# Kernel tuning notes

Measured on AMD Instinct MI355X. Metric: run time of the kernel, lower is better.

The kernel has to match this reference:

```python
import jax, jax.numpy as jnp
import numpy as np

G, S, M = 131072, 16, 8  # num_groups, state_dim, measure_dim


def setup_inputs() -> dict:
    key = jax.random.key(0)
    ks = jax.random.split(key, 7)
    inp = jax.random.normal(ks[0], (G, M), jnp.float32)
    mean = jax.random.normal(ks[1], (G, S), jnp.float32)
    a = jax.random.normal(ks[2], (G, S, S), jnp.float32)
    cov = a @ jnp.swapaxes(a, -1, -2) / S + jnp.eye(S, dtype=jnp.float32)  # SPD state cov
    H = jax.random.normal(ks[3], (G, M, S), jnp.float32) * 0.5
    b = jax.random.normal(ks[4], (G, M, M), jnp.float32)
    R = b @ jnp.swapaxes(b, -1, -2) / M + jnp.eye(M, dtype=jnp.float32)  # SPD measure noise
    F = jax.random.normal(ks[5], (G, S, S), jnp.float32) * (0.5 / np.sqrt(S))  # quasi-stable transition
    c = jax.random.normal(ks[6], (G, S, S), jnp.float32)
    Q = c @ jnp.swapaxes(c, -1, -2) / S + 0.1 * jnp.eye(S, dtype=jnp.float32)  # SPD process noise
    return {"input": inp, "mean": mean, "cov": cov, "H": H, "R": R, "F": F, "Q": Q}


def reference(input, mean, cov, H, R, F, Q):
    # --- update (no-NaN path of GaussianStep.update -> _update) ---
    Ht = jnp.swapaxes(H, -1, -2)                     # [G,S,M]
    covHt = cov @ Ht                                 # [G,S,M]
    Ssys = H @ covHt + R                             # innovation covariance [G,M,M]
    # torch: solve(B=covHt^T, A=Ssys^T) then transpose -> K = covHt @ inv(Ssys)
    Kt = jnp.linalg.solve(jnp.swapaxes(Ssys, -1, -2), jnp.swapaxes(covHt, -1, -2))  # [G,M,S]
    K = jnp.swapaxes(Kt, -1, -2)                     # [G,S,M]
    resid = input - jnp.einsum('gms,gs->gm', H, mean)
    new_mean = mean + jnp.einsum('gsm,gm->gs', K, resid)
    I = jnp.eye(S, dtype=cov.dtype)
    ikh = I - K @ H                                  # [G,S,S]
    # stable (Joseph form) covariance update
    new_cov = ikh @ cov @ jnp.swapaxes(ikh, -1, -2) + K @ R @ jnp.swapaxes(K, -1, -2)
    # --- predict ---
    pred_mean = jnp.einsum('gij,gj->gi', F, new_mean)
    pred_cov = F @ new_cov @ jnp.swapaxes(F, -1, -2) + Q
    return pred_mean, pred_cov
```

## Files before the change

### kernel.cpp

```cpp
#include <hip/hip_runtime.h>


typedef float v2f __attribute__((ext_vector_type(2)));
typedef _Float16 h2 __attribute__((ext_vector_type(2)));

__device__ __forceinline__ float bq(float x, int t) {
    switch (t & 3) {
    case 0:  return __int_as_float(__builtin_amdgcn_mov_dpp(__float_as_int(x), 0x00, 0xF, 0xF, true));
    case 1:  return __int_as_float(__builtin_amdgcn_mov_dpp(__float_as_int(x), 0x55, 0xF, 0xF, true));
    case 2:  return __int_as_float(__builtin_amdgcn_mov_dpp(__float_as_int(x), 0xAA, 0xF, 0xF, true));
    default: return __int_as_float(__builtin_amdgcn_mov_dpp(__float_as_int(x), 0xFF, 0xF, 0xF, true));
    }
}
__device__ __forceinline__ v2f splat(float c) { v2f r; r.x = c; r.y = c; return r; }
__device__ __forceinline__ v2f up2(h2 h) { v2f r; r.x = (float)h.x; r.y = (float)h.y; return r; }

__global__ __launch_bounds__(64) void kalman_kernel(
    const float* __restrict__ g_in,
    const float* __restrict__ g_mean,
    const float* __restrict__ g_cov,
    const float* __restrict__ g_H,
    const float* __restrict__ g_R,
    const float* __restrict__ g_F,
    const float* __restrict__ g_Q,
    float* __restrict__ g_out,
    int G)
{
    const int l = threadIdx.x & 3;
    const int g = (blockIdx.x << 4) | (threadIdx.x >> 2);

    const float* const Pp = g_cov + (size_t)g * 256;
    const float* const Hp = g_H   + (size_t)g * 128;
    const float* const Rp = g_R   + (size_t)g * 64;
    const float* const Fp = g_F   + (size_t)g * 256;
    const float* const Qp = g_Q   + (size_t)g * 256;

    v2f Plo[16], Phi[16];
    #pragma unroll
    for (int k = 0; k < 16; ++k) {
        const float4 t = *reinterpret_cast<const float4*>(Pp + k*16 + 4*l);
        Plo[k].x=t.x; Plo[k].y=t.y; Phi[k].x=t.z; Phi[k].y=t.w;
    }
    h2 HT16[16];
    {
        float4 ra[4], rb[4];
        #pragma unroll
        for (int p = 0; p < 4; ++p) {
            ra[p] = *reinterpret_cast<const float4*>(Hp + (2*l  )*16 + 4*p);
            rb[p] = *reinterpret_cast<const float4*>(Hp + (2*l+1)*16 + 4*p);
        }
        #pragma unroll
        for (int p = 0; p < 4; ++p) {
            HT16[4*p+0].x=(_Float16)ra[p].x; HT16[4*p+0].y=(_Float16)rb[p].x;
            HT16[4*p+1].x=(_Float16)ra[p].y; HT16[4*p+1].y=(_Float16)rb[p].y;
            HT16[4*p+2].x=(_Float16)ra[p].z; HT16[4*p+2].y=(_Float16)rb[p].z;
            HT16[4*p+3].x=(_Float16)ra[p].w; HT16[4*p+3].y=(_Float16)rb[p].w;
        }
    }
    v2f S[8];
    #pragma unroll
    for (int i = 0; i < 8; ++i) {
        const float2 t = *reinterpret_cast<const float2*>(Rp + i*8 + 2*l);
        S[i].x=t.x; S[i].y=t.y;
    }
    v2f mnlo, mnhi;
    { const float4 t = *reinterpret_cast<const float4*>(g_mean + (size_t)g*16 + 4*l);
      mnlo.x=t.x; mnlo.y=t.y; mnhi.x=t.z; mnhi.y=t.w; }
    v2f ipv;
    { const float2 t = *reinterpret_cast<const float2*>(g_in + (size_t)g*8 + 2*l);
      ipv.x=t.x; ipv.y=t.y; }

    v2f CTlo[8], CThi[8];
    #pragma unroll
    for (int i = 0; i < 8; ++i) {
        v2f alo = {0.f, 0.f}, ahi = {0.f, 0.f};
        #pragma unroll
        for (int k = 0; k < 16; ++k) {
            const float h = bq((float)((i&1) ? HT16[k].y : HT16[k].x), i>>1);
            alo += splat(h) * Plo[k];
            ahi += splat(h) * Phi[k];
        }
        CTlo[i]=alo; CThi[i]=ahi;
    }

    #pragma unroll
    for (int i = 0; i < 8; ++i) {
        v2f acc = S[i];
        #pragma unroll
        for (int k = 0; k < 16; ++k) {
            const float c = bq((k&2) ? ((k&1)?CThi[i].y:CThi[i].x)
                                     : ((k&1)?CTlo[i].y:CTlo[i].x), k>>2);
            acc += splat(c) * up2(HT16[k]);
        }
        S[i] = acc;
    }

    v2f resd = ipv;
    #pragma unroll
    for (int k = 0; k < 16; ++k) {
        const float m = bq((k&2) ? ((k&1)?mnhi.y:mnhi.x)
                                 : ((k&1)?mnlo.y:mnlo.x), k>>2);
        resd -= splat(m) * up2(HT16[k]);
    }

    v2f Ii[8];
    #pragma unroll
    for (int i = 0; i < 8; ++i) {
        Ii[i].x = (2*l   == i) ? 1.f : 0.f;
        Ii[i].y = (2*l+1 == i) ? 1.f : 0.f;
    }
    #pragma unroll
    for (int k = 0; k < 8; ++k) {
        const float pv   = bq((k&1) ? S[k].y : S[k].x, k>>1);
        const float pinv = __builtin_amdgcn_rcpf(pv);
        S[k]  *= splat(pinv);
        Ii[k] *= splat(pinv);
        #pragma unroll
        for (int i = 0; i < 8; ++i) {
            if (i == k) continue;
            const float fi = bq((k&1) ? S[i].y : S[i].x, k>>1);
            S[i]  -= splat(fi) * S[k];
            Ii[i] -= splat(fi) * Ii[k];
        }
    }

    h2 FT16a[16], FT16b[16];
    {
        #pragma unroll
        for (int p = 0; p < 4; ++p) {
            const float4 r0 = *reinterpret_cast<const float4*>(Fp + (4*l+0)*16 + 4*p);
            const float4 r1 = *reinterpret_cast<const float4*>(Fp + (4*l+1)*16 + 4*p);
            const float4 r2 = *reinterpret_cast<const float4*>(Fp + (4*l+2)*16 + 4*p);
            const float4 r3 = *reinterpret_cast<const float4*>(Fp + (4*l+3)*16 + 4*p);
            FT16a[4*p+0].x=(_Float16)r0.x; FT16a[4*p+0].y=(_Float16)r1.x;
            FT16b[4*p+0].x=(_Float16)r2.x; FT16b[4*p+0].y=(_Float16)r3.x;
            FT16a[4*p+1].x=(_Float16)r0.y; FT16a[4*p+1].y=(_Float16)r1.y;
            FT16b[4*p+1].x=(_Float16)r2.y; FT16b[4*p+1].y=(_Float16)r3.y;
            FT16a[4*p+2].x=(_Float16)r0.z; FT16a[4*p+2].y=(_Float16)r1.z;
            FT16b[4*p+2].x=(_Float16)r2.z; FT16b[4*p+2].y=(_Float16)r3.z;
            FT16a[4*p+3].x=(_Float16)r0.w; FT16a[4*p+3].y=(_Float16)r1.w;
            FT16b[4*p+3].x=(_Float16)r2.w; FT16b[4*p+3].y=(_Float16)r3.w;
        }
    }

    v2f nmL = mnlo, nmH = mnhi;
    #pragma unroll
    for (int m = 0; m < 8; ++m) {
        v2f xlo = {0.f,0.f}, xhi = {0.f,0.f};
        #pragma unroll
        for (int j = 0; j < 8; ++j) {
            const float s = bq((j&1) ? Ii[m].y : Ii[m].x, j>>1);
            xlo += splat(s) * CTlo[j];
            xhi += splat(s) * CThi[j];
        }
        const float r = bq((m&1) ? resd.y : resd.x, m>>1);
        nmL += splat(r) * xlo;
        nmH += splat(r) * xhi;
        #pragma unroll
        for (int s2 = 0; s2 < 16; ++s2) {
            const float c = bq((s2&2) ? ((s2&1)?CThi[m].y:CThi[m].x)
                                      : ((s2&1)?CTlo[m].y:CTlo[m].x), s2>>2);
            Plo[s2] -= splat(c) * xlo;
            Phi[s2] -= splat(c) * xhi;
        }
    }

    {
        v2f plo = {0.f,0.f}, phi = {0.f,0.f};
        #pragma unroll
        for (int k = 0; k < 16; ++k) {
            const float m = bq((k&2) ? ((k&1)?nmH.y:nmH.x)
                                     : ((k&1)?nmL.y:nmL.x), k>>2);
            plo += splat(m) * up2(FT16a[k]);
            phi += splat(m) * up2(FT16b[k]);
        }
        *reinterpret_cast<float4*>(g_out + (size_t)g*16 + 4*l) =
            make_float4(plo.x, plo.y, phi.x, phi.y);
    }

    float* const out_pc = g_out + (size_t)G*16 + (size_t)g*256;
    #pragma unroll
    for (int i = 0; i < 16; ++i) {
        const float4 qv = *reinterpret_cast<const float4*>(Qp + i*16 + 4*l);
        v2f wlo = {0.f,0.f}, whi = {0.f,0.f};
        #pragma unroll
        for (int k = 0; k < 16; ++k) {
            const float f = bq((float)((i&2) ? ((i&1)?FT16b[k].y:FT16b[k].x)
                                             : ((i&1)?FT16a[k].y:FT16a[k].x)), i>>2);
            wlo += splat(f) * Plo[k];
            whi += splat(f) * Phi[k];
        }
        v2f olo; olo.x=qv.x; olo.y=qv.y;
        v2f ohi; ohi.x=qv.z; ohi.y=qv.w;
        #pragma unroll
        for (int t = 0; t < 16; ++t) {
            const float wb = bq((t&2) ? ((t&1)?whi.y:whi.x)
                                      : ((t&1)?wlo.y:wlo.x), t>>2);
            olo += splat(wb) * up2(FT16a[t]);
            ohi += splat(wb) * up2(FT16b[t]);
        }
        *reinterpret_cast<float4*>(out_pc + i*16 + 4*l) =
            make_float4(olo.x, olo.y, ohi.x, ohi.y);
    }
}

extern "C" void kernel_launch(void* const* d_in, const int* in_sizes, int n_in,
                              void* d_out, int out_size, void* d_ws, size_t ws_size,
                              hipStream_t stream) {
    const float* g_in   = (const float*)d_in[0];
    const float* g_mean = (const float*)d_in[1];
    const float* g_cov  = (const float*)d_in[2];
    const float* g_H    = (const float*)d_in[3];
    const float* g_R    = (const float*)d_in[4];
    const float* g_F    = (const float*)d_in[5];
    const float* g_Q    = (const float*)d_in[6];
    float* out = (float*)d_out;
    const int G = in_sizes[2] / 256;
    kalman_kernel<<<G/16, 64, 0, stream>>>(g_in, g_mean, g_cov, g_H, g_R, g_F, g_Q, out, G);
}
```

Baseline: 158.3 us.

## Process two groups per thread quad with software-prefetched loads for second group

Each block now handles 32 groups: every thread quad processes group A, then group B, and during group A's output loop it prefetches group B's cov, H, R, mean and input into registers, with sched barriers placing the loads. Q is also loaded through a 5-deep rotating register buffer, and H is kept in fp32 instead of being converted to fp16. The aim is to hide global-load latency behind compute and cut launch overhead. The cost is much higher register pressure, which may lower occupancy or cause spills, and half as many blocks.

```diff
diff --git a/kernel.cpp b/kernel.cpp
--- a/kernel.cpp
+++ b/kernel.cpp
@@ -26,181 +26,375 @@
     float* __restrict__ g_out,
     int G)
 {
-    const int l = threadIdx.x & 3;
-    const int g = (blockIdx.x << 4) | (threadIdx.x >> 2);
-
-    const float* const Pp = g_cov + (size_t)g * 256;
-    const float* const Hp = g_H   + (size_t)g * 128;
-    const float* const Rp = g_R   + (size_t)g * 64;
-    const float* const Fp = g_F   + (size_t)g * 256;
-    const float* const Qp = g_Q   + (size_t)g * 256;
-
-    v2f Plo[16], Phi[16];
-    #pragma unroll
-    for (int k = 0; k < 16; ++k) {
-        const float4 t = *reinterpret_cast<const float4*>(Pp + k*16 + 4*l);
-        Plo[k].x=t.x; Plo[k].y=t.y; Phi[k].x=t.z; Phi[k].y=t.w;
+    const int l  = threadIdx.x & 3;
+    const int gA = (blockIdx.x << 5) | (threadIdx.x >> 2);
+    const int gB = gA + 16;
+
+    float4 tPB[16];
+    float4 tHaB[4], tHbB[4];
+    float2 tSB[8];
+    float4 tmnB;
+    float2 tipB;
+
+    float* const out_pc_base = g_out + (size_t)G * 16;
+
+    {
+        const float* const Pp = g_cov + (size_t)gA * 256;
+        const float* const Hp = g_H   + (size_t)gA * 128;
+        const float* const Rp = g_R   + (size_t)gA * 64;
+        const float* const Fp = g_F   + (size_t)gA * 256;
+        const float* const Qp = g_Q   + (size_t)gA * 256;
+
+        v2f Plo[16], Phi[16];
+        #pragma unroll
+        for (int k = 0; k < 16; ++k) {
+            const float4 t = *reinterpret_cast<const float4*>(Pp + k*16 + 4*l);
+            Plo[k].x=t.x; Plo[k].y=t.y; Phi[k].x=t.z; Phi[k].y=t.w;
+        }
+        v2f HT[16];
+        {
+            float4 ra[4], rb[4];
+            #pragma unroll
+            for (int p = 0; p < 4; ++p) {
+                ra[p] = *reinterpret_cast<const float4*>(Hp + (2*l  )*16 + 4*p);
+                rb[p] = *reinterpret_cast<const float4*>(Hp + (2*l+1)*16 + 4*p);
+            }
+            #pragma unroll
+            for (int p = 0; p < 4; ++p) {
+                HT[4*p+0].x=ra[p].x; HT[4*p+0].y=rb[p].x;
+                HT[4*p+1].x=ra[p].y; HT[4*p+1].y=rb[p].y;
+                HT[4*p+2].x=ra[p].z; HT[4*p+2].y=rb[p].z;
+                HT[4*p+3].x=ra[p].w; HT[4*p+3].y=rb[p].w;
+            }
+        }
+        v2f S[8];
+        #pragma unroll
+        for (int i = 0; i < 8; ++i) {
+            const float2 t = *reinterpret_cast<const float2*>(Rp + i*8 + 2*l);
+            S[i].x=t.x; S[i].y=t.y;
+        }
+        v2f mnlo, mnhi;
+        { const float4 t = *reinterpret_cast<const float4*>(g_mean + (size_t)gA*16 + 4*l);
+          mnlo.x=t.x; mnlo.y=t.y; mnhi.x=t.z; mnhi.y=t.w; }
+        v2f ipv;
+        { const float2 t = *reinterpret_cast<const float2*>(g_in + (size_t)gA*8 + 2*l);
+          ipv.x=t.x; ipv.y=t.y; }
+
+        v2f CTlo[8], CThi[8];
+        #pragma unroll
+        for (int i = 0; i < 8; ++i) {
+            v2f alo = {0.f,0.f}, ahi = {0.f,0.f};
+            #pragma unroll
+            for (int k = 0; k < 16; ++k) {
+                const float h = bq((i&1) ? HT[k].y : HT[k].x, i>>1);
+                alo += splat(h) * Plo[k];
+                ahi += splat(h) * Phi[k];
+            }
+            CTlo[i]=alo; CThi[i]=ahi;
+        }
+        #pragma unroll
+        for (int i = 0; i < 8; ++i) {
+            v2f acc = S[i];
+            #pragma unroll
+            for (int k = 0; k < 16; ++k) {
+                const float c = bq((k&2) ? ((k&1)?CThi[i].y:CThi[i].x)
+                                         : ((k&1)?CTlo[i].y:CTlo[i].x), k>>2);
+                acc += splat(c) * HT[k];
+            }
+            S[i] = acc;
+        }
+        v2f resd = ipv;
+        #pragma unroll
+        for (int k = 0; k < 16; ++k) {
+            const float m = bq((k&2) ? ((k&1)?mnhi.y:mnhi.x)
+                                     : ((k&1)?mnlo.y:mnlo.x), k>>2);
+            resd -= splat(m) * HT[k];
+        }
+        v2f Ii[8];
+        #pragma unroll
+        for (int i = 0; i < 8; ++i) {
+            Ii[i].x = (2*l   == i) ? 1.f : 0.f;
+            Ii[i].y = (2*l+1 == i) ? 1.f : 0.f;
+        }
+        #pragma unroll
+        for (int k = 0; k < 8; ++k) {
+            const float pv   = bq((k&1) ? S[k].y : S[k].x, k>>1);
+            const float pinv = __builtin_amdgcn_rcpf(pv);
+            S[k]  *= splat(pinv);
+            Ii[k] *= splat(pinv);
+            #pragma unroll
+            for (int i = 0; i < 8; ++i) {
+                if (i == k) continue;
+                const float fi = bq((k&1) ? S[i].y : S[i].x, k>>1);
+                S[i]  -= splat(fi) * S[k];
+                Ii[i] -= splat(fi) * Ii[k];
+            }
+        }
+        h2 FT16a[16], FT16b[16];
+        {
+            #pragma unroll
+            for (int p = 0; p < 4; ++p) {
+                const float4 r0 = *reinterpret_cast<const float4*>(Fp + (4*l+0)*16 + 4*p);
+                const float4 r1 = *reinterpret_cast<const float4*>(Fp + (4*l+1)*16 + 4*p);
+                const float4 r2 = *reinterpret_cast<const float4*>(Fp + (4*l+2)*16 + 4*p);
+                const float4 r3 = *reinterpret_cast<const float4*>(Fp + (4*l+3)*16 + 4*p);
+                FT16a[4*p+0].x=(_Float16)r0.x; FT16a[4*p+0].y=(_Float16)r1.x;
+                FT16b[4*p+0].x=(_Float16)r2.x; FT16b[4*p+0].y=(_Float16)r3.x;
+                FT16a[4*p+1].x=(_Float16)r0.y; FT16a[4*p+1].y=(_Float16)r1.y;
+                FT16b[4*p+1].x=(_Float16)r2.y; FT16b[4*p+1].y=(_Float16)r3.y;
+                FT16a[4*p+2].x=(_Float16)r0.z; FT16a[4*p+2].y=(_Float16)r1.z;
+                FT16b[4*p+2].x=(_Float16)r2.z; FT16b[4*p+2].y=(_Float16)r3.z;
+                FT16a[4*p+3].x=(_Float16)r0.w; FT16a[4*p+3].y=(_Float16)r1.w;
+                FT16b[4*p+3].x=(_Float16)r2.w; FT16b[4*p+3].y=(_Float16)r3.w;
+            }
+        }
+        float4 qbuf[5];
+        #pragma unroll
+        for (int i = 0; i < 5; ++i)
+            qbuf[i] = *reinterpret_cast<const float4*>(Qp + i*16 + 4*l);
+
+        v2f nmL = mnlo, nmH = mnhi;
+        #pragma unroll
+        for (int m = 0; m < 8; ++m) {
+            v2f xlo = {0.f,0.f}, xhi = {0.f,0.f};
+            #pragma unroll
+            for (int j = 0; j < 8; ++j) {
+                const float s = bq((j&1) ? Ii[m].y : Ii[m].x, j>>1);
+                xlo += splat(s) * CTlo[j];
+                xhi += splat(s) * CThi[j];
+            }
+            const float r = bq((m&1) ? resd.y : resd.x, m>>1);
+            nmL += splat(r) * xlo;
+            nmH += splat(r) * xhi;
+            #pragma unroll
+            for (int s2 = 0; s2 < 16; ++s2) {
+                const float c = bq((s2&2) ? ((s2&1)?CThi[m].y:CThi[m].x)
+                                          : ((s2&1)?CTlo[m].y:CTlo[m].x), s2>>2);
+                Plo[s2] -= splat(c) * xlo;
+                Phi[s2] -= splat(c) * xhi;
+            }
+        }
+        {
+            v2f plo = {0.f,0.f}, phi = {0.f,0.f};
+            #pragma unroll
+            for (int k = 0; k < 16; ++k) {
+                const float m = bq((k&2) ? ((k&1)?nmH.y:nmH.x)
+                                         : ((k&1)?nmL.y:nmL.x), k>>2);
+                plo += splat(m) * up2(FT16a[k]);
+                phi += splat(m) * up2(FT16b[k]);
+            }
+            *reinterpret_cast<float4*>(g_out + (size_t)gA*16 + 4*l) =
+                make_float4(plo.x, plo.y, phi.x, phi.y);
+        }
+        const float* const PpB = g_cov + (size_t)gB * 256;
+        const float* const HpB = g_H   + (size_t)gB * 128;
+        const float* const RpB = g_R   + (size_t)gB * 64;
+        float* const out_pc = out_pc_base + (size_t)gA*256;
+        #pragma unroll
+        for (int i = 0; i < 16; ++i) {
+            v2f wlo = {0.f,0.f}, whi = {0.f,0.f};
+            #pragma unroll
+            for (int k = 0; k < 16; ++k) {
+                const float f = bq((float)((i&2) ? ((i&1)?FT16b[k].y:FT16b[k].x)
+                                                 : ((i&1)?FT16a[k].y:FT16a[k].x)), i>>2);
+                wlo += splat(f) * Plo[k];
+                whi += splat(f) * Phi[k];
+            }
+            const float4 qv = qbuf[i % 5];
+            if (i + 5 < 16)
+                qbuf[i % 5] = *reinterpret_cast<const float4*>(Qp + (i+5)*16 + 4*l);
+            v2f olo; olo.x=qv.x; olo.y=qv.y;
+            v2f ohi; ohi.x=qv.z; ohi.y=qv.w;
+            #pragma unroll
+            for (int t = 0; t < 16; ++t) {
+                const float wb = bq((t&2) ? ((t&1)?whi.y:whi.x)
+                                          : ((t&1)?wlo.y:wlo.x), t>>2);
+                olo += splat(wb) * up2(FT16a[t]);
+                ohi += splat(wb) * up2(FT16b[t]);
+            }
+            *reinterpret_cast<float4*>(out_pc + i*16 + 4*l) =
+                make_float4(olo.x, olo.y, ohi.x, ohi.y);
+            if (i == 2) {
+                #pragma unroll
+                for (int k = 0; k < 16; ++k)
+                    tPB[k] = *reinterpret_cast<const float4*>(PpB + k*16 + 4*l);
+                __builtin_amdgcn_sched_barrier(0);
+            }
+            if (i == 6) {
+                #pragma unroll
+                for (int p = 0; p < 4; ++p) {
+                    tHaB[p] = *reinterpret_cast<const float4*>(HpB + (2*l  )*16 + 4*p);
+                    tHbB[p] = *reinterpret_cast<const float4*>(HpB + (2*l+1)*16 + 4*p);
+                }
+                __builtin_amdgcn_sched_barrier(0);
+            }
+            if (i == 10) {
+                #pragma unroll
+                for (int r = 0; r < 8; ++r)
+                    tSB[r] = *reinterpret_cast<const float2*>(RpB + r*8 + 2*l);
+                tmnB = *reinterpret_cast<const float4*>(g_mean + (size_t)gB*16 + 4*l);
+                tipB = *reinterpret_cast<const float2*>(g_in + (size_t)gB*8 + 2*l);
+                __builtin_amdgcn_sched_barrier(0);
+            }
+        }
     }
-    h2 HT16[16];
+
     {
-        float4 ra[4], rb[4];
+        const float* const Fp = g_F + (size_t)gB * 256;
+        const float* const Qp = g_Q + (size_t)gB * 256;
+
+        v2f Plo[16], Phi[16];
+        #pragma unroll
+        for (int k = 0; k < 16; ++k) {
+            Plo[k].x=tPB[k].x; Plo[k].y=tPB[k].y; Phi[k].x=tPB[k].z; Phi[k].y=tPB[k].w;
+        }
+        v2f HT[16];
         #pragma unroll
         for (int p = 0; p < 4; ++p) {
-            ra[p] = *reinterpret_cast<const float4*>(Hp + (2*l  )*16 + 4*p);
-            rb[p] = *reinterpret_cast<const float4*>(Hp + (2*l+1)*16 + 4*p);
-        }
-        #pragma unroll
-        for (int p = 0; p < 4; ++p) {
-            HT16[4*p+0].x=(_Float16)ra[p].x; HT16[4*p+0].y=(_Float16)rb[p].x;
-            HT16[4*p+1].x=(_Float16)ra[p].y; HT16[4*p+1].y=(_Float16)rb[p].y;
-            HT16[4*p+2].x=(_Float16)ra[p].z; HT16[4*p+2].y=(_Float16)rb[p].z;
-            HT16[4*p+3].x=(_Float16)ra[p].w; HT16[4*p+3].y=(_Float16)rb[p].w;
-        }
-    }
-    v2f S[8];
-    #pragma unroll
-    for (int i = 0; i < 8; ++i) {
-        const float2 t = *reinterpret_cast<const float2*>(Rp + i*8 + 2*l);
-        S[i].x=t.x; S[i].y=t.y;
-    }
-    v2f mnlo, mnhi;
-    { const float4 t = *reinterpret_cast<const float4*>(g_mean + (size_t)g*16 + 4*l);
-      mnlo.x=t.x; mnlo.y=t.y; mnhi.x=t.z; mnhi.y=t.w; }
-    v2f ipv;
-    { const float2 t = *reinterpret_cast<const float2*>(g_in + (size_t)g*8 + 2*l);
-      ipv.x=t.x; ipv.y=t.y; }
-
-    v2f CTlo[8], CThi[8];
-    #pragma unroll
-    for (int i = 0; i < 8; ++i) {
-        v2f alo = {0.f, 0.f}, ahi = {0.f, 0.f};
+            HT[4*p+0].x=tHaB[p].x; HT[4*p+0].y=tHbB[p].x;
+            HT[4*p+1].x=tHaB[p].y; HT[4*p+1].y=tHbB[p].y;
+            HT[4*p+2].x=tHaB[p].z; HT[4*p+2].y=tHbB[p].z;
+            HT[4*p+3].x=tHaB[p].w; HT[4*p+3].y=tHbB[p].w;
+        }
+        v2f S[8];
+        #pragma unroll
+        for (int i = 0; i < 8; ++i) { S[i].x=tSB[i].x; S[i].y=tSB[i].y; }
+        v2f mnlo, mnhi;
+        mnlo.x=tmnB.x; mnlo.y=tmnB.y; mnhi.x=tmnB.z; mnhi.y=tmnB.w;
+        v2f ipv; ipv.x=tipB.x; ipv.y=tipB.y;
+
+        v2f CTlo[8], CThi[8];
+        #pragma unroll
+        for (int i = 0; i < 8; ++i) {
+            v2f alo = {0.f,0.f}, ahi = {0.f,0.f};
+            #pragma unroll
+            for (int k = 0; k < 16; ++k) {
+                const float h = bq((i&1) ? HT[k].y : HT[k].x, i>>1);
+                alo += splat(h) * Plo[k];
+                ahi += splat(h) * Phi[k];
+            }
+            CTlo[i]=alo; CThi[i]=ahi;
+        }
+        #pragma unroll
+        for (int i = 0; i < 8; ++i) {
+            v2f acc = S[i];
+            #pragma unroll
+            for (int k = 0; k < 16; ++k) {
+                const float c = bq((k&2) ? ((k&1)?CThi[i].y:CThi[i].x)
+                                         : ((k&1)?CTlo[i].y:CTlo[i].x), k>>2);
+                acc += splat(c) * HT[k];
+            }
+            S[i] = acc;
+        }
+        v2f resd = ipv;
         #pragma unroll
         for (int k = 0; k < 16; ++k) {
-            const float h = bq((float)((i&1) ? HT16[k].y : HT16[k].x), i>>1);
-            alo += splat(h) * Plo[k];
-            ahi += splat(h) * Phi[k];
-        }
-        CTlo[i]=alo; CThi[i]=ahi;
-    }
-
-    #pragma unroll
-    for (int i = 0; i < 8; ++i) {
-        v2f acc = S[i];
-        #pragma unroll
-        for (int k = 0; k < 16; ++k) {
-            const float c = bq((k&2) ? ((k&1)?CThi[i].y:CThi[i].x)
-                                     : ((k&1)?CTlo[i].y:CTlo[i].x), k>>2);
-            acc += splat(c) * up2(HT16[k]);
-        }
-        S[i] = acc;
-    }
-
-    v2f resd = ipv;
-    #pragma unroll
-    for (int k = 0; k < 16; ++k) {
-        const float m = bq((k&2) ? ((k&1)?mnhi.y:mnhi.x)
-                                 : ((k&1)?mnlo.y:mnlo.x), k>>2);
-        resd -= splat(m) * up2(HT16[k]);
-    }
-
-    v2f Ii[8];
-    #pragma unroll
-    for (int i = 0; i < 8; ++i) {
-        Ii[i].x = (2*l   == i) ? 1.f : 0.f;
-        Ii[i].y = (2*l+1 == i) ? 1.f : 0.f;
-    }
-    #pragma unroll
-    for (int k = 0; k < 8; ++k) {
-        const float pv   = bq((k&1) ? S[k].y : S[k].x, k>>1);
-        const float pinv = __builtin_amdgcn_rcpf(pv);
-        S[k]  *= splat(pinv);
-        Ii[k] *= splat(pinv);
-        #pragma unroll
-        for (int i = 0; i < 8; ++i) {
-            if (i == k) continue;
-            const float fi = bq((k&1) ? S[i].y : S[i].x, k>>1);
-            S[i]  -= splat(fi) * S[k];
-            Ii[i] -= splat(fi) * Ii[k];
-        }
-    }
-
-    h2 FT16a[16], FT16b[16];
-    {
-        #pragma unroll
-        for (int p = 0; p < 4; ++p) {
-            const float4 r0 = *reinterpret_cast<const float4*>(Fp + (4*l+0)*16 + 4*p);
-            const float4 r1 = *reinterpret_cast<const float4*>(Fp + (4*l+1)*16 + 4*p);
-            const float4 r2 = *reinterpret_cast<const float4*>(Fp + (4*l+2)*16 + 4*p);
-            const float4 r3 = *reinterpret_cast<const float4*>(Fp + (4*l+3)*16 + 4*p);
-            FT16a[4*p+0].x=(_Float16)r0.x; FT16a[4*p+0].y=(_Float16)r1.x;
-            FT16b[4*p+0].x=(_Float16)r2.x; FT16b[4*p+0].y=(_Float16)r3.x;
-            FT16a[4*p+1].x=(_Float16)r0.y; FT16a[4*p+1].y=(_Float16)r1.y;
-            FT16b[4*p+1].x=(_Float16)r2.y; FT16b[4*p+1].y=(_Float16)r3.y;
-            FT16a[4*p+2].x=(_Float16)r0.z; FT16a[4*p+2].y=(_Float16)r1.z;
-            FT16b[4*p+2].x=(_Float16)r2.z; FT16b[4*p+2].y=(_Float16)r3.z;
-            FT16a[4*p+3].x=(_Float16)r0.w; FT16a[4*p+3].y=(_Float16)r1.w;
-            FT16b[4*p+3].x=(_Float16)r2.w; FT16b[4*p+3].y=(_Float16)r3.w;
-        }
-    }
-
-    v2f nmL = mnlo, nmH = mnhi;
-    #pragma unroll
-    for (int m = 0; m < 8; ++m) {
-        v2f xlo = {0.f,0.f}, xhi = {0.f,0.f};
-        #pragma unroll
-        for (int j = 0; j < 8; ++j) {
-            const float s = bq((j&1) ? Ii[m].y : Ii[m].x, j>>1);
-            xlo += splat(s) * CTlo[j];
-            xhi += splat(s) * CThi[j];
-        }
-        const float r = bq((m&1) ? resd.y : resd.x, m>>1);
-        nmL += splat(r) * xlo;
-        nmH += splat(r) * xhi;
-        #pragma unroll
-        for (int s2 = 0; s2 < 16; ++s2) {
-            const float c = bq((s2&2) ? ((s2&1)?CThi[m].y:CThi[m].x)
-                                      : ((s2&1)?CTlo[m].y:CTlo[m].x), s2>>2);
-            Plo[s2] -= splat(c) * xlo;
-            Phi[s2] -= splat(c) * xhi;
-        }
-    }
-
-    {
-        v2f plo = {0.f,0.f}, phi = {0.f,0.f};
-        #pragma unroll
-        for (int k = 0; k < 16; ++k) {
-            const float m = bq((k&2) ? ((k&1)?nmH.y:nmH.x)
-                                     : ((k&1)?nmL.y:nmL.x), k>>2);
-            plo += splat(m) * up2(FT16a[k]);
-            phi += splat(m) * up2(FT16b[k]);
-        }
-        *reinterpret_cast<float4*>(g_out + (size_t)g*16 + 4*l) =
-            make_float4(plo.x, plo.y, phi.x, phi.y);
-    }
-
-    float* const out_pc = g_out + (size_t)G*16 + (size_t)g*256;
-    #pragma unroll
-    for (int i = 0; i < 16; ++i) {
-        const float4 qv = *reinterpret_cast<const float4*>(Qp + i*16 + 4*l);
-        v2f wlo = {0.f,0.f}, whi = {0.f,0.f};
-        #pragma unroll
-        for (int k = 0; k < 16; ++k) {
-            const float f = bq((float)((i&2) ? ((i&1)?FT16b[k].y:FT16b[k].x)
-                                             : ((i&1)?FT16a[k].y:FT16a[k].x)), i>>2);
-            wlo += splat(f) * Plo[k];
-            whi += splat(f) * Phi[k];
-        }
-        v2f olo; olo.x=qv.x; olo.y=qv.y;
-        v2f ohi; ohi.x=qv.z; ohi.y=qv.w;
-        #pragma unroll
-        for (int t = 0; t < 16; ++t) {
-            const float wb = bq((t&2) ? ((t&1)?whi.y:whi.x)
-                                      : ((t&1)?wlo.y:wlo.x), t>>2);
-            olo += splat(wb) * up2(FT16a[t]);
-            ohi += splat(wb) * up2(FT16b[t]);
-        }
-        *reinterpret_cast<float4*>(out_pc + i*16 + 4*l) =
-            make_float4(olo.x, olo.y, ohi.x, ohi.y);
+            const float m = bq((k&2) ? ((k&1)?mnhi.y:mnhi.x)
+                                     : ((k&1)?mnlo.y:mnlo.x), k>>2);
+            resd -= splat(m) * HT[k];
+        }
+        v2f Ii[8];
+        #pragma unroll
+        for (int i = 0; i < 8; ++i) {
+            Ii[i].x = (2*l   == i) ? 1.f : 0.f;
+            Ii[i].y = (2*l+1 == i) ? 1.f : 0.f;
+        }
+        #pragma unroll
+        for (int k = 0; k < 8; ++k) {
+            const float pv   = bq((k&1) ? S[k].y : S[k].x, k>>1);
+            const float pinv = __builtin_amdgcn_rcpf(pv);
+            S[k]  *= splat(pinv);
+            Ii[k] *= splat(pinv);
+            #pragma unroll
+            for (int i = 0; i < 8; ++i) {
+                if (i == k) continue;
+                const float fi = bq((k&1) ? S[i].y : S[i].x, k>>1);
+                S[i]  -= splat(fi) * S[k];
+                Ii[i] -= splat(fi) * Ii[k];
+            }
+        }
+        h2 FT16a[16], FT16b[16];
+        {
+            #pragma unroll
+            for (int p = 0; p < 4; ++p) {
+                const float4 r0 = *reinterpret_cast<const float4*>(Fp + (4*l+0)*16 + 4*p);
+                const float4 r1 = *reinterpret_cast<const float4*>(Fp + (4*l+1)*16 + 4*p);
+                const float4 r2 = *reinterpret_cast<const float4*>(Fp + (4*l+2)*16 + 4*p);
+                const float4 r3 = *reinterpret_cast<const float4*>(Fp + (4*l+3)*16 + 4*p);
+                FT16a[4*p+0].x=(_Float16)r0.x; FT16a[4*p+0].y=(_Float16)r1.x;
+                FT16b[4*p+0].x=(_Float16)r2.x; FT16b[4*p+0].y=(_Float16)r3.x;
+                FT16a[4*p+1].x=(_Float16)r0.y; FT16a[4*p+1].y=(_Float16)r1.y;
+                FT16b[4*p+1].x=(_Float16)r2.y; FT16b[4*p+1].y=(_Float16)r3.y;
+                FT16a[4*p+2].x=(_Float16)r0.z; FT16a[4*p+2].y=(_Float16)r1.z;
+                FT16b[4*p+2].x=(_Float16)r2.z; FT16b[4*p+2].y=(_Float16)r3.z;
+                FT16a[4*p+3].x=(_Float16)r0.w; FT16a[4*p+3].y=(_Float16)r1.w;
+                FT16b[4*p+3].x=(_Float16)r2.w; FT16b[4*p+3].y=(_Float16)r3.w;
+            }
+        }
+        float4 qbuf[5];
+        #pragma unroll
+        for (int i = 0; i < 5; ++i)
+            qbuf[i] = *reinterpret_cast<const float4*>(Qp + i*16 + 4*l);
+
+        v2f nmL = mnlo, nmH = mnhi;
+        #pragma unroll
+        for (int m = 0; m < 8; ++m) {
+            v2f xlo = {0.f,0.f}, xhi = {0.f,0.f};
+            #pragma unroll
+            for (int j = 0; j < 8; ++j) {
+                const float s = bq((j&1) ? Ii[m].y : Ii[m].x, j>>1);
+                xlo += splat(s) * CTlo[j];
+                xhi += splat(s) * CThi[j];
+            }
+            const float r = bq((m&1) ? resd.y : resd.x, m>>1);
+            nmL += splat(r) * xlo;
+            nmH += splat(r) * xhi;
+            #pragma unroll
+            for (int s2 = 0; s2 < 16; ++s2) {
+                const float c = bq((s2&2) ? ((s2&1)?CThi[m].y:CThi[m].x)
+                                          : ((s2&1)?CTlo[m].y:CTlo[m].x), s2>>2);
+                Plo[s2] -= splat(c) * xlo;
+                Phi[s2] -= splat(c) * xhi;
+            }
+        }
+        {
+            v2f plo = {0.f,0.f}, phi = {0.f,0.f};
+            #pragma unroll
+            for (int k = 0; k < 16; ++k) {
+                const float m = bq((k&2) ? ((k&1)?nmH.y:nmH.x)
+                                         : ((k&1)?nmL.y:nmL.x), k>>2);
+                plo += splat(m) * up2(FT16a[k]);
+                phi += splat(m) * up2(FT16b[k]);
+            }
+            *reinterpret_cast<float4*>(g_out + (size_t)gB*16 + 4*l) =
+                make_float4(plo.x, plo.y, phi.x, phi.y);
+        }
+        float* const out_pc = out_pc_base + (size_t)gB*256;
+        #pragma unroll
+        for (int i = 0; i < 16; ++i) {
+            v2f wlo = {0.f,0.f}, whi = {0.f,0.f};
+            #pragma unroll
+            for (int k = 0; k < 16; ++k) {
+                const float f = bq((float)((i&2) ? ((i&1)?FT16b[k].y:FT16b[k].x)
+                                                 : ((i&1)?FT16a[k].y:FT16a[k].x)), i>>2);
+                wlo += splat(f) * Plo[k];
+                whi += splat(f) * Phi[k];
+            }
+            const float4 qv = qbuf[i % 5];
+            if (i + 5 < 16)
+                qbuf[i % 5] = *reinterpret_cast<const float4*>(Qp + (i+5)*16 + 4*l);
+            v2f olo; olo.x=qv.x; olo.y=qv.y;
+            v2f ohi; ohi.x=qv.z; ohi.y=qv.w;
+            #pragma unroll
+            for (int t = 0; t < 16; ++t) {
+                const float wb = bq((t&2) ? ((t&1)?whi.y:whi.x)
+                                          : ((t&1)?wlo.y:wlo.x), t>>2);
+                olo += splat(wb) * up2(FT16a[t]);
+                ohi += splat(wb) * up2(FT16b[t]);
+            }
+            *reinterpret_cast<float4*>(out_pc + i*16 + 4*l) =
+                make_float4(olo.x, olo.y, ohi.x, ohi.y);
+        }
     }
 }
 
@@ -216,5 +410,5 @@
     const float* g_Q    = (const float*)d_in[6];
     float* out = (float*)d_out;
     const int G = in_sizes[2] / 256;
-    kalman_kernel<<<G/16, 64, 0, stream>>>(g_in, g_mean, g_cov, g_H, g_R, g_F, g_Q, out, G);
+    kalman_kernel<<<G/32, 64, 0, stream>>>(g_in, g_mean, g_cov, g_H, g_R, g_F, g_Q, out, G);
 }
```

Result: faster. 140.2 us (-11.4%).

## Invert innovation matrix in place and reorder loads to cut register pressure

Applied to the files above, without the earlier changes.

Replaces the separate Gauss-Jordan identity array with in-place inversion inside S, so the explicit inverse shares storage with the matrix being reduced. The residual is computed early and the mean reloaded later instead of being held live. R is loaded lazily, a sched_barrier keeps the F loads after the update phase, and Q rows are prefetched two ahead. The aim is fewer live VGPRs, which may allow higher occupancy or avoid spills. The cost is some extra select instructions and a repeated mean load.

```diff
diff --git a/kernel.cpp b/kernel.cpp
--- a/kernel.cpp
+++ b/kernel.cpp
@@ -57,23 +57,22 @@
             HT16[4*p+3].x=(_Float16)ra[p].w; HT16[4*p+3].y=(_Float16)rb[p].w;
         }
     }
-    v2f S[8];
+    v2f resd;
+    {
+        const float2 it = *reinterpret_cast<const float2*>(g_in + (size_t)g*8 + 2*l);
+        const float4 mt = *reinterpret_cast<const float4*>(g_mean + (size_t)g*16 + 4*l);
+        resd.x = it.x; resd.y = it.y;
+        #pragma unroll
+        for (int k = 0; k < 16; ++k) {
+            const float m = bq((k&2) ? ((k&1)?mt.w:mt.z) : ((k&1)?mt.y:mt.x), k>>2);
+            resd -= splat(m) * up2(HT16[k]);
+        }
+    }
+
+    v2f CTlo[8], CThi[8];
     #pragma unroll
     for (int i = 0; i < 8; ++i) {
-        const float2 t = *reinterpret_cast<const float2*>(Rp + i*8 + 2*l);
-        S[i].x=t.x; S[i].y=t.y;
-    }
-    v2f mnlo, mnhi;
-    { const float4 t = *reinterpret_cast<const float4*>(g_mean + (size_t)g*16 + 4*l);
-      mnlo.x=t.x; mnlo.y=t.y; mnhi.x=t.z; mnhi.y=t.w; }
-    v2f ipv;
-    { const float2 t = *reinterpret_cast<const float2*>(g_in + (size_t)g*8 + 2*l);
-      ipv.x=t.x; ipv.y=t.y; }
-
-    v2f CTlo[8], CThi[8];
-    #pragma unroll
-    for (int i = 0; i < 8; ++i) {
-        v2f alo = {0.f, 0.f}, ahi = {0.f, 0.f};
+        v2f alo = {0.f,0.f}, ahi = {0.f,0.f};
         #pragma unroll
         for (int k = 0; k < 16; ++k) {
             const float h = bq((float)((i&1) ? HT16[k].y : HT16[k].x), i>>1);
@@ -83,9 +82,11 @@
         CTlo[i]=alo; CThi[i]=ahi;
     }
 
+    v2f S[8];
     #pragma unroll
     for (int i = 0; i < 8; ++i) {
-        v2f acc = S[i];
+        const float2 rt = *reinterpret_cast<const float2*>(Rp + i*8 + 2*l);
+        v2f acc; acc.x = rt.x; acc.y = rt.y;
         #pragma unroll
         for (int k = 0; k < 16; ++k) {
             const float c = bq((k&2) ? ((k&1)?CThi[i].y:CThi[i].x)
@@ -95,34 +96,50 @@
         S[i] = acc;
     }
 
-    v2f resd = ipv;
-    #pragma unroll
-    for (int k = 0; k < 16; ++k) {
-        const float m = bq((k&2) ? ((k&1)?mnhi.y:mnhi.x)
-                                 : ((k&1)?mnlo.y:mnlo.x), k>>2);
-        resd -= splat(m) * up2(HT16[k]);
-    }
-
-    v2f Ii[8];
-    #pragma unroll
-    for (int i = 0; i < 8; ++i) {
-        Ii[i].x = (2*l   == i) ? 1.f : 0.f;
-        Ii[i].y = (2*l+1 == i) ? 1.f : 0.f;
-    }
     #pragma unroll
     for (int k = 0; k < 8; ++k) {
-        const float pv   = bq((k&1) ? S[k].y : S[k].x, k>>1);
-        const float pinv = __builtin_amdgcn_rcpf(pv);
-        S[k]  *= splat(pinv);
-        Ii[k] *= splat(pinv);
+        const float p    = bq((k&1) ? S[k].y : S[k].x, k>>1);
+        const float pinv = __builtin_amdgcn_rcpf(p);
+        S[k] *= splat(pinv);
+        S[k].x = (2*l   == k) ? pinv : S[k].x;
+        S[k].y = (2*l+1 == k) ? pinv : S[k].y;
         #pragma unroll
         for (int i = 0; i < 8; ++i) {
             if (i == k) continue;
-            const float fi = bq((k&1) ? S[i].y : S[i].x, k>>1);
-            S[i]  -= splat(fi) * S[k];
-            Ii[i] -= splat(fi) * Ii[k];
-        }
-    }
+            const float f  = bq((k&1) ? S[i].y : S[i].x, k>>1);
+            const float nf = -f * pinv;
+            S[i] -= splat(f) * S[k];
+            S[i].x = (2*l   == k) ? nf : S[i].x;
+            S[i].y = (2*l+1 == k) ? nf : S[i].y;
+        }
+    }
+
+    v2f nmL, nmH;
+    {
+        const float4 mt = *reinterpret_cast<const float4*>(g_mean + (size_t)g*16 + 4*l);
+        nmL.x=mt.x; nmL.y=mt.y; nmH.x=mt.z; nmH.y=mt.w;
+    }
+    #pragma unroll
+    for (int m = 0; m < 8; ++m) {
+        v2f xlo = {0.f,0.f}, xhi = {0.f,0.f};
+        #pragma unroll
+        for (int j = 0; j < 8; ++j) {
+            const float s = bq((j&1) ? S[m].y : S[m].x, j>>1);
+            xlo += splat(s) * CTlo[j];
+            xhi += splat(s) * CThi[j];
+        }
+        const float r = bq((m&1) ? resd.y : resd.x, m>>1);
+        nmL += splat(r) * xlo;
+        nmH += splat(r) * xhi;
+        #pragma unroll
+        for (int s2 = 0; s2 < 16; ++s2) {
+            const float c = bq((s2&2) ? ((s2&1)?CThi[m].y:CThi[m].x)
+                                      : ((s2&1)?CTlo[m].y:CTlo[m].x), s2>>2);
+            Plo[s2] -= splat(c) * xlo;
+            Phi[s2] -= splat(c) * xhi;
+        }
+    }
+    __builtin_amdgcn_sched_barrier(0);
 
     h2 FT16a[16], FT16b[16];
     {
@@ -143,28 +160,6 @@
         }
     }
 
-    v2f nmL = mnlo, nmH = mnhi;
-    #pragma unroll
-    for (int m = 0; m < 8; ++m) {
-        v2f xlo = {0.f,0.f}, xhi = {0.f,0.f};
-        #pragma unroll
-        for (int j = 0; j < 8; ++j) {
-            const float s = bq((j&1) ? Ii[m].y : Ii[m].x, j>>1);
-            xlo += splat(s) * CTlo[j];
-            xhi += splat(s) * CThi[j];
-        }
-        const float r = bq((m&1) ? resd.y : resd.x, m>>1);
-        nmL += splat(r) * xlo;
-        nmH += splat(r) * xhi;
-        #pragma unroll
-        for (int s2 = 0; s2 < 16; ++s2) {
-            const float c = bq((s2&2) ? ((s2&1)?CThi[m].y:CThi[m].x)
-                                      : ((s2&1)?CTlo[m].y:CTlo[m].x), s2>>2);
-            Plo[s2] -= splat(c) * xlo;
-            Phi[s2] -= splat(c) * xhi;
-        }
-    }
-
     {
         v2f plo = {0.f,0.f}, phi = {0.f,0.f};
         #pragma unroll
@@ -179,9 +174,12 @@
     }
 
     float* const out_pc = g_out + (size_t)G*16 + (size_t)g*256;
+    float4 qbuf[2];
+    #pragma unroll
+    for (int i = 0; i < 2; ++i)
+        qbuf[i] = *reinterpret_cast<const float4*>(Qp + i*16 + 4*l);
     #pragma unroll
     for (int i = 0; i < 16; ++i) {
-        const float4 qv = *reinterpret_cast<const float4*>(Qp + i*16 + 4*l);
         v2f wlo = {0.f,0.f}, whi = {0.f,0.f};
         #pragma unroll
         for (int k = 0; k < 16; ++k) {
@@ -190,6 +188,9 @@
             wlo += splat(f) * Plo[k];
             whi += splat(f) * Phi[k];
         }
+        const float4 qv = qbuf[i & 1];
+        if (i + 2 < 16)
+            qbuf[i & 1] = *reinterpret_cast<const float4*>(Qp + (i+2)*16 + 4*l);
         v2f olo; olo.x=qv.x; olo.y=qv.y;
         v2f ohi; ohi.x=qv.z; ohi.y=qv.w;
         #pragma unroll
```

Result: faster. 147.2 us (-7.0%).
